# Optimization experiments

Hardware: AMD Instinct MI355X
Metric: run time of the kernel (lower is better)

Reference implementation:

```python
import jax, jax.numpy as jnp
import numpy as np

B, M, D, N, P = 8, 4096, 1024, 64, 2
TEMP = 0.1
EPS = 1e-12  # torch F.normalize default eps


def setup_inputs() -> dict:
    key = jax.random.key(0)
    k1, k2, k3 = jax.random.split(key, 3)
    x = jax.random.normal(k1, (B, M, D), jnp.float32)
    # xavier_normal_(phi, gain=1.5): std = 1.5*sqrt(2/(fan_in+fan_out)) with fan_in=D, fan_out=N*P
    phi = jax.random.normal(k2, (D, N, P), jnp.float32) * np.float32(1.5 * np.sqrt(2.0 / (D + N * P)))
    scale = jnp.ones((1,), jnp.float32)
    W = jax.random.normal(k3, (N, D, D), jnp.float32) * np.float32(1.0 / np.sqrt(D))
    b = jnp.zeros((N, D), jnp.float32)
    return {"x": x, "phi": phi, "scale": scale, "W": W, "b": b}


def reference(x, phi, scale, W, b):
    # normalize tokens along feature dim, phi along dim 0 (like F.normalize)
    xn = x / jnp.maximum(jnp.linalg.norm(x, axis=2, keepdims=True), EPS)
    phin = scale * (phi / jnp.maximum(jnp.linalg.norm(phi, axis=0, keepdims=True), EPS))
    # router logits [b, m, n, p]
    logits = jnp.einsum('bmd,dnp->bmnp', xn, phin) / TEMP
    d = jax.nn.softmax(logits, axis=1)                    # dispatch: softmax over tokens m
    c = jax.nn.softmax(logits.reshape(B, M, N * P), axis=-1).reshape(B, M, N, P)  # combine: softmax over (n,p)
    xs = jnp.einsum('bmd,bmnp->bnpd', x, d)               # slot inputs [b, n, p, d]
    # per-expert Linear(dim, dim): batched over expert axis n
    ys = jnp.einsum('bnpd,nde->bnpe', xs, W) + b[None, :, None, :]
    y = jnp.einsum('bnpd,bmnp->bmd', ys, c)
    return y + x  # add_residual=True
```

## Files before the change

kernel.cpp:

```cpp
#include <hip/hip_runtime.h>
#include <hip/hip_bf16.h>
#include <math.h>

#define B_ 8
#define M_ 4096
#define D_ 1024
#define NP_ 128
#define TEMP_ 0.1f
#define EPS_ 1e-12f

typedef __attribute__((ext_vector_type(8))) short bf16x8;
typedef __attribute__((ext_vector_type(4))) float f32x4;

__device__ __forceinline__ unsigned short f2bf(float f) {
    union { float f; unsigned int u; } v; v.f = f;
    unsigned int u = v.u;
    u += 0x7fff + ((u >> 16) & 1);
    return (unsigned short)(u >> 16);
}

__device__ __forceinline__ void stage_tile(const char* gbase, size_t row_stride,
                                           char* lds, int tid) {
    const int lane = tid & 63, w = tid >> 6;
#pragma unroll
    for (int t = 0; t < 2; ++t) {
        const int row = w * 32 + t * 16 + (lane >> 2);
        const char* g = gbase + (size_t)row * row_stride + (lane & 3) * 16;
        char* l = lds + (w * 32 + t * 16) * 64 + lane * 16;
        __builtin_amdgcn_global_load_lds((const __attribute__((address_space(1))) unsigned int*)g,
                                         (__attribute__((address_space(3))) unsigned int*)l,
                                         16, 0, 0);
    }
}

__device__ __forceinline__ void stage_rows64(const char* gbase, size_t row_stride,
                                             char* lds, int tid) {
    const int lane = tid & 63, w = tid >> 6;
    const int row = w * 16 + (lane >> 2);
    const char* g = gbase + (size_t)row * row_stride + (lane & 3) * 16;
    char* l = lds + (w * 16) * 64 + lane * 16;
    __builtin_amdgcn_global_load_lds((const __attribute__((address_space(1))) unsigned int*)g,
                                     (__attribute__((address_space(3))) unsigned int*)l,
                                     16, 0, 0);
}

template <int NI, int NJ>
__device__ __forceinline__ void mfma_tile(const char* At, const char* Bt,
                                          f32x4 (&acc)[NI][NJ], int wm, int wn,
                                          int fr, int q) {
    bf16x8 a[NI], bb[NJ];
#pragma unroll
    for (int i = 0; i < NI; ++i)
        a[i] = *(const bf16x8*)(At + (wm + i * 16 + fr) * 64 + q * 16);
#pragma unroll
    for (int j = 0; j < NJ; ++j)
        bb[j] = *(const bf16x8*)(Bt + (wn + j * 16 + fr) * 64 + q * 16);
#pragma unroll
    for (int i = 0; i < NI; ++i)
#pragma unroll
        for (int j = 0; j < NJ; ++j)
            acc[i][j] = __builtin_amdgcn_mfma_f32_16x16x32_bf16(a[i], bb[j], acc[i][j], 0, 0, 0);
}

__global__ __launch_bounds__(256) void k_prepT(const float* __restrict__ x,
                                               unsigned short* __restrict__ xbf,
                                               unsigned short* __restrict__ xbfT,
                                               float* __restrict__ rinv) {
    const int p = blockIdx.x;
    const int b = p >> 6, m0 = (p & 63) * 64;
    const int tid = threadIdx.x;
    const int mg = tid >> 4;
    const int d4 = tid & 15;
    __shared__ unsigned short lt[2][64][72];
    float ss[4] = {0.f, 0.f, 0.f, 0.f};
    for (int ch = 0; ch < 16; ++ch) {
        const int d0 = ch * 64;
        const int buf = ch & 1;
#pragma unroll
        for (int ii = 0; ii < 4; ++ii) {
            const int m = mg + ii * 16;
            float4 v = *(const float4*)(x + ((size_t)(b * M_ + m0 + m)) * D_ + d0 + d4 * 4);
            ss[ii] += v.x * v.x + v.y * v.y + v.z * v.z + v.w * v.w;
            ushort4 bv;
            bv.x = f2bf(v.x); bv.y = f2bf(v.y); bv.z = f2bf(v.z); bv.w = f2bf(v.w);
            *(ushort4*)(xbf + ((size_t)(b * M_ + m0 + m)) * D_ + d0 + d4 * 4) = bv;
            lt[buf][d4 * 4 + 0][m] = bv.x;
            lt[buf][d4 * 4 + 1][m] = bv.y;
            lt[buf][d4 * 4 + 2][m] = bv.z;
            lt[buf][d4 * 4 + 3][m] = bv.w;
        }
        __syncthreads();
        const int dl = tid >> 2, mq = (tid & 3) * 16;
        bf16x8 v0 = *(const bf16x8*)&lt[buf][dl][mq];
        bf16x8 v1 = *(const bf16x8*)&lt[buf][dl][mq + 8];
        unsigned short* to = xbfT + ((size_t)(b * D_ + d0 + dl)) * M_ + m0 + mq;
        *(bf16x8*)(to) = v0;
        *(bf16x8*)(to + 8) = v1;
    }
#pragma unroll
    for (int ii = 0; ii < 4; ++ii) {
        float s = ss[ii];
        s += __shfl_down(s, 8, 16);
        s += __shfl_down(s, 4, 16);
        s += __shfl_down(s, 2, 16);
        s += __shfl_down(s, 1, 16);
        if (d4 == 0)
            rinv[b * M_ + m0 + mg + ii * 16] = 1.0f / (fmaxf(sqrtf(s), EPS_) * TEMP_);
    }
}

__global__ void k_phin(const float* __restrict__ phi, const float* __restrict__ scale,
                       unsigned short* __restrict__ phinT) {
    const int np = blockIdx.x, tid = threadIdx.x;
    float ss = 0.f;
    for (int d = tid; d < D_; d += 256) {
        float v = phi[d * NP_ + np];
        ss += v * v;
    }
    __shared__ float red[256];
    red[tid] = ss;
    __syncthreads();
    for (int s = 128; s > 0; s >>= 1) {
        if (tid < s) red[tid] += red[tid + s];
        __syncthreads();
    }
    float inv = scale[0] / fmaxf(sqrtf(red[0]), EPS_);
    for (int d = tid; d < D_; d += 256) phinT[np * D_ + d] = f2bf(phi[d * NP_ + np] * inv);
}

__global__ __launch_bounds__(256) void k_logits(const unsigned short* __restrict__ phinT,
                                                const unsigned short* __restrict__ xbf,
                                                const float* __restrict__ rinv,
                                                float* __restrict__ logitsT) {
    const int b = blockIdx.y, m0 = blockIdx.x * 64;
    const int tid = threadIdx.x, lane = tid & 63, w = tid >> 6;
    __shared__ char At[2][8192], Bt[2][4096];
    f32x4 acc[4][2] = {};
    const char* abase = (const char*)phinT;
    const char* bbase = (const char*)(xbf + ((size_t)b * M_ + m0) * D_);
    const int wm = (w & 1) * 64, wn = (w >> 1) * 32;
    const int fr = lane & 15, q = lane >> 4;
    stage_tile(abase, 2048, At[0], tid);
    stage_rows64(bbase, 2048, Bt[0], tid);
    __syncthreads();
    int cur = 0;
    for (int k0 = 64; k0 < 2048; k0 += 64) {
        stage_tile(abase + k0, 2048, At[cur ^ 1], tid);
        stage_rows64(bbase + k0, 2048, Bt[cur ^ 1], tid);
        mfma_tile<4, 2>(At[cur], Bt[cur], acc, wm, wn, fr, q);
        __syncthreads();
        cur ^= 1;
    }
    mfma_tile<4, 2>(At[cur], Bt[cur], acc, wm, wn, fr, q);
#pragma unroll
    for (int j = 0; j < 2; ++j) {
        const int m = m0 + wn + j * 16 + fr;
        const float r = rinv[b * M_ + m];
#pragma unroll
        for (int i = 0; i < 4; ++i) {
            const int nprow = wm + i * 16 + q * 4;
#pragma unroll
            for (int reg = 0; reg < 4; ++reg)
                logitsT[((size_t)b * NP_ + nprow + reg) * M_ + m] = acc[i][j][reg] * r;
        }
    }
}

__global__ void k_colstats(const float* __restrict__ logitsT, float* __restrict__ cmax,
                           float* __restrict__ cinv) {
    const int row = blockIdx.x * 4 + (threadIdx.x >> 6);
    const int lane = threadIdx.x & 63;
    const float4* base = (const float4*)(logitsT + (size_t)row * M_);
    float mx = -1e30f, sm = 0.f;
#pragma unroll 4
    for (int it = 0; it < 16; ++it) {
        float4 v = base[lane + 64 * it];
        float lm = fmaxf(fmaxf(v.x, v.y), fmaxf(v.z, v.w));
        float nm = fmaxf(mx, lm);
        sm = sm * __expf(mx - nm) + __expf(v.x - nm) + __expf(v.y - nm) + __expf(v.z - nm) +
             __expf(v.w - nm);
        mx = nm;
    }
    for (int off = 32; off > 0; off >>= 1) {
        float om = __shfl_down(mx, off), os = __shfl_down(sm, off);
        float nm = fmaxf(mx, om);
        sm = sm * __expf(mx - nm) + os * __expf(om - nm);
        mx = nm;
    }
    if (lane == 0) {
        cmax[row] = mx;
        cinv[row] = 1.0f / sm;
    }
}

__global__ __launch_bounds__(256) void k_weights(const float* __restrict__ logitsT,
                                                 const float* __restrict__ cmax,
                                                 const float* __restrict__ cinv,
                                                 unsigned short* __restrict__ dvalT,
                                                 unsigned short* __restrict__ cbf) {
    const int b = blockIdx.y, m0 = blockIdx.x * 32;
    const int tid = threadIdx.x;
    __shared__ float lt[128][36];
    __shared__ float red[32][8];
    __shared__ float rstat[32][2];
    const int np = tid >> 1;
    const int mh = (tid & 1) * 16;
    const float cm = cmax[b * NP_ + np], ci = cinv[b * NP_ + np];
#pragma unroll
    for (int ii = 0; ii < 4; ++ii) {
        const int mq = mh + ii * 4;
        float4 v = *(const float4*)(logitsT + ((size_t)b * NP_ + np) * M_ + m0 + mq);
        *(float4*)&lt[np][mq] = v;
        ushort4 e;
        e.x = f2bf(__expf(v.x - cm) * ci);
        e.y = f2bf(__expf(v.y - cm) * ci);
        e.z = f2bf(__expf(v.z - cm) * ci);
        e.w = f2bf(__expf(v.w - cm) * ci);
        *(ushort4*)(dvalT + ((size_t)b * NP_ + np) * M_ + m0 + mq) = e;
    }
    __syncthreads();
    const int mm = tid >> 3, g = tid & 7;
    float mx = -1e30f;
#pragma unroll
    for (int i = 0; i < 16; ++i) mx = fmaxf(mx, lt[g * 16 + i][mm]);
    red[mm][g] = mx;
    __syncthreads();
    if (g == 0) {
        float M2 = red[mm][0];
#pragma unroll
        for (int k = 1; k < 8; ++k) M2 = fmaxf(M2, red[mm][k]);
        rstat[mm][0] = M2;
    }
    __syncthreads();
    const float rm = rstat[mm][0];
    float s = 0.f;
#pragma unroll
    for (int i = 0; i < 16; ++i) s += __expf(lt[g * 16 + i][mm] - rm);
    red[mm][g] = s;
    __syncthreads();
    if (g == 0) {
        float S = 0.f;
#pragma unroll
        for (int k = 0; k < 8; ++k) S += red[mm][k];
        rstat[mm][1] = 1.0f / S;
    }
    __syncthreads();
    const float ri = rstat[mm][1];
    bf16x8 o0, o1;
#pragma unroll
    for (int i = 0; i < 8; ++i) o0[i] = (short)f2bf(__expf(lt[g * 16 + i][mm] - rm) * ri);
#pragma unroll
    for (int i = 0; i < 8; ++i) o1[i] = (short)f2bf(__expf(lt[g * 16 + 8 + i][mm] - rm) * ri);
    unsigned short* co = cbf + ((size_t)b * M_ + m0 + mm) * NP_ + g * 16;
    *(bf16x8*)(co) = o0;
    *(bf16x8*)(co + 8) = o1;
}

__global__ __launch_bounds__(256) void k_xs(const unsigned short* __restrict__ dvalT,
                                            const unsigned short* __restrict__ xbfT,
                                            float* __restrict__ partial) {
    const int dt = blockIdx.x, kc = blockIdx.y, b = blockIdx.z;
    const int d0 = dt * 128;
    const int tid = threadIdx.x, lane = tid & 63, w = tid >> 6;
    __shared__ char At[2][8192], Bt[2][8192];
    f32x4 acc[4][4] = {};
    const char* abase = (const char*)(dvalT + (size_t)b * NP_ * M_) + (size_t)kc * 1024;
    const char* bbase = (const char*)(xbfT + ((size_t)b * D_ + d0) * M_) + (size_t)kc * 1024;
    const int wm = (w & 1) * 64, wn = (w >> 1) * 64;
    const int fr = lane & 15, q = lane >> 4;
    stage_tile(abase, (size_t)M_ * 2, At[0], tid);
    stage_tile(bbase, (size_t)M_ * 2, Bt[0], tid);
    __syncthreads();
    int cur = 0;
    for (int k0 = 64; k0 < 1024; k0 += 64) {
        stage_tile(abase + k0, (size_t)M_ * 2, At[cur ^ 1], tid);
        stage_tile(bbase + k0, (size_t)M_ * 2, Bt[cur ^ 1], tid);
        mfma_tile<4, 4>(At[cur], Bt[cur], acc, wm, wn, fr, q);
        __syncthreads();
        cur ^= 1;
    }
    mfma_tile<4, 4>(At[cur], Bt[cur], acc, wm, wn, fr, q);
#pragma unroll
    for (int j = 0; j < 4; ++j) {
        const int d = d0 + wn + j * 16 + fr;
#pragma unroll
        for (int i = 0; i < 4; ++i) {
            const int nprow = wm + i * 16 + q * 4;
#pragma unroll
            for (int reg = 0; reg < 4; ++reg)
                partial[(((size_t)kc * B_ + b) * NP_ + nprow + reg) * D_ + d] = acc[i][j][reg];
        }
    }
}

__global__ void k_xsred(const float* __restrict__ partial, float* __restrict__ xs) {
    const size_t i = ((size_t)blockIdx.x * 256 + threadIdx.x) * 4;
    const size_t CH = (size_t)B_ * NP_ * D_;
    float4 o = *(const float4*)(partial + i);
#pragma unroll
    for (int c = 1; c < 8; ++c) {
        float4 s = *(const float4*)(partial + (size_t)c * CH + i);
        o.x += s.x; o.y += s.y; o.z += s.z; o.w += s.w;
    }
    *(float4*)(xs + i) = o;
}

__global__ __launch_bounds__(256) void k_ys(const float* __restrict__ xs,
                                            const float* __restrict__ W,
                                            const float* __restrict__ bias,
                                            unsigned short* __restrict__ ysT) {
    const int et = blockIdx.x;
    const int n = blockIdx.y;
    const int e0 = et * 128;
    const int tid = threadIdx.x, tx = tid & 31, ty = tid >> 5;
    __shared__ float wt[32][128];
    __shared__ float xst[16][32];
    float acc[2][4];
#pragma unroll
    for (int j = 0; j < 2; ++j)
#pragma unroll
        for (int q = 0; q < 4; ++q) acc[j][q] = 0.f;
    const float* wbase = W + (size_t)n * D_ * D_;
    for (int k0 = 0; k0 < D_; k0 += 32) {
#pragma unroll
        for (int it = 0; it < 4; ++it) {
            int idx = tid + 256 * it;
            int row = idx >> 5, c4 = (idx & 31) * 4;
            *(float4*)(&wt[row][c4]) = *(const float4*)(wbase + (size_t)(k0 + row) * D_ + e0 + c4);
        }
        if (tid < 128) {
            int r = tid >> 3, c4 = (tid & 7) * 4;
            int bb = r >> 1, pp = r & 1;
            *(float4*)(&xst[r][c4]) =
                *(const float4*)(xs + ((size_t)bb * NP_ + n * 2 + pp) * D_ + k0 + c4);
        }
        __syncthreads();
#pragma unroll
        for (int k = 0; k < 32; ++k) {
            float4 w4 = *(const float4*)(&wt[k][tx * 4]);
            float r0 = xst[ty * 2][k], r1 = xst[ty * 2 + 1][k];
            acc[0][0] += r0 * w4.x; acc[0][1] += r0 * w4.y;
            acc[0][2] += r0 * w4.z; acc[0][3] += r0 * w4.w;
            acc[1][0] += r1 * w4.x; acc[1][1] += r1 * w4.y;
            acc[1][2] += r1 * w4.z; acc[1][3] += r1 * w4.w;
        }
        __syncthreads();
    }
    float4 bv = *(const float4*)(bias + n * D_ + e0 + tx * 4);
#pragma unroll
    for (int j = 0; j < 2; ++j) {
        const int r = ty * 2 + j;
        const int bb = r >> 1, pp = r & 1;
        float v0 = acc[j][0] + bv.x, v1 = acc[j][1] + bv.y;
        float v2 = acc[j][2] + bv.z, v3 = acc[j][3] + bv.w;
        ysT[((size_t)bb * D_ + e0 + tx * 4 + 0) * NP_ + n * 2 + pp] = f2bf(v0);
        ysT[((size_t)bb * D_ + e0 + tx * 4 + 1) * NP_ + n * 2 + pp] = f2bf(v1);
        ysT[((size_t)bb * D_ + e0 + tx * 4 + 2) * NP_ + n * 2 + pp] = f2bf(v2);
        ysT[((size_t)bb * D_ + e0 + tx * 4 + 3) * NP_ + n * 2 + pp] = f2bf(v3);
    }
}

__global__ __launch_bounds__(256) void k_final(const unsigned short* __restrict__ cbf,
                                               const unsigned short* __restrict__ ysT,
                                               const float* __restrict__ x,
                                               float* __restrict__ out) {
    const int et = blockIdx.x, mt = blockIdx.y, b = blockIdx.z;
    const int e0 = et * 128, m0 = mt * 128;
    const int tid = threadIdx.x, lane = tid & 63, w = tid >> 6;
    __shared__ char At[2][8192], Bt[2][8192];
    f32x4 acc[4][4] = {};
    const char* abase = (const char*)(cbf + ((size_t)b * M_ + m0) * NP_);
    const char* bbase = (const char*)(ysT + ((size_t)b * D_ + e0) * NP_);
    const int wm = (w & 1) * 64, wn = (w >> 1) * 64;
    const int fr = lane & 15, q = lane >> 4;
    stage_tile(abase, 256, At[0], tid);
    stage_tile(bbase, 256, Bt[0], tid);
    __syncthreads();
    int cur = 0;
    for (int k0 = 64; k0 < 256; k0 += 64) {
        stage_tile(abase + k0, 256, At[cur ^ 1], tid);
        stage_tile(bbase + k0, 256, Bt[cur ^ 1], tid);
        mfma_tile<4, 4>(At[cur], Bt[cur], acc, wm, wn, fr, q);
        __syncthreads();
        cur ^= 1;
    }
    mfma_tile<4, 4>(At[cur], Bt[cur], acc, wm, wn, fr, q);
#pragma unroll
    for (int i = 0; i < 4; ++i) {
#pragma unroll
        for (int reg = 0; reg < 4; ++reg) {
            const int m = m0 + wm + i * 16 + q * 4 + reg;
#pragma unroll
            for (int j = 0; j < 4; ++j) {
                const int e = e0 + wn + j * 16 + fr;
                const size_t idx = ((size_t)b * M_ + m) * D_ + e;
                out[idx] = acc[i][j][reg] + x[idx];
            }
        }
    }
}

extern "C" void kernel_launch(void* const* d_in, const int* in_sizes, int n_in,
                              void* d_out, int out_size, void* d_ws, size_t ws_size,
                              hipStream_t stream) {
    const float* x = (const float*)d_in[0];
    const float* phi = (const float*)d_in[1];
    const float* scale = (const float*)d_in[2];
    const float* W = (const float*)d_in[3];
    const float* bias = (const float*)d_in[4];
    float* out = (float*)d_out;

    char* ws = (char*)d_ws;
    float* rinv = (float*)ws;
    float* cmax = (float*)(ws + 131072);
    float* cinv = (float*)(ws + 135168);
    unsigned short* phinT = (unsigned short*)(ws + 139264);
    unsigned short* xbf = (unsigned short*)(ws + 401408);
    unsigned short* xbfT = (unsigned short*)(ws + 401408 + 67108864);
    float* logitsT = (float*)(ws + 401408 + 134217728);
    unsigned short* dvalT = (unsigned short*)(ws + 401408 + 150994944);
    unsigned short* cbf = (unsigned short*)(ws + 401408 + 159383552);
    float* partial = (float*)xbf;
    float* xs = (float*)((char*)xbf + 33554432);
    unsigned short* ysT = (unsigned short*)((char*)xbf + 37748736);

    k_prepT<<<512, 256, 0, stream>>>(x, xbf, xbfT, rinv);
    k_phin<<<128, 256, 0, stream>>>(phi, scale, phinT);
    k_logits<<<dim3(64, 8), 256, 0, stream>>>(phinT, xbf, rinv, logitsT);
    k_colstats<<<256, 256, 0, stream>>>(logitsT, cmax, cinv);
    k_weights<<<dim3(128, 8), 256, 0, stream>>>(logitsT, cmax, cinv, dvalT, cbf);
    k_xs<<<dim3(8, 8, 8), 256, 0, stream>>>(dvalT, xbfT, partial);
    k_xsred<<<1024, 256, 0, stream>>>(partial, xs);
    k_ys<<<dim3(8, 64), 256, 0, stream>>>(xs, W, bias, ysT);
    k_final<<<dim3(8, 32, 8), 256, 0, stream>>>(cbf, ysT, x, out);
}
```

Baseline: 661.1 us.

## Swap GEMM operand roles for vectorized float4 epilogue stores and split logits grid

```diff
diff --git a/kernel.cpp b/kernel.cpp
--- a/kernel.cpp
+++ b/kernel.cpp
@@ -132,36 +132,41 @@
                                                 const unsigned short* __restrict__ xbf,
                                                 const float* __restrict__ rinv,
                                                 float* __restrict__ logitsT) {
-    const int b = blockIdx.y, m0 = blockIdx.x * 64;
+    const int m0 = blockIdx.x * 64;
+    const int np0 = blockIdx.y * 64;
+    const int b = blockIdx.z;
     const int tid = threadIdx.x, lane = tid & 63, w = tid >> 6;
-    __shared__ char At[2][8192], Bt[2][4096];
-    f32x4 acc[4][2] = {};
-    const char* abase = (const char*)phinT;
-    const char* bbase = (const char*)(xbf + ((size_t)b * M_ + m0) * D_);
-    const int wm = (w & 1) * 64, wn = (w >> 1) * 32;
+    __shared__ char At[2][4096], Bt[2][4096];
+    f32x4 acc[2][2] = {};
+    const char* abase = (const char*)(xbf + ((size_t)b * M_ + m0) * D_);
+    const char* bbase = (const char*)(phinT + (size_t)np0 * D_);
+    const int wmm = (w & 1) * 32, wnn = (w >> 1) * 32;
     const int fr = lane & 15, q = lane >> 4;
-    stage_tile(abase, 2048, At[0], tid);
+    stage_rows64(abase, 2048, At[0], tid);
     stage_rows64(bbase, 2048, Bt[0], tid);
     __syncthreads();
     int cur = 0;
     for (int k0 = 64; k0 < 2048; k0 += 64) {
-        stage_tile(abase + k0, 2048, At[cur ^ 1], tid);
+        stage_rows64(abase + k0, 2048, At[cur ^ 1], tid);
         stage_rows64(bbase + k0, 2048, Bt[cur ^ 1], tid);
-        mfma_tile<4, 2>(At[cur], Bt[cur], acc, wm, wn, fr, q);
+        mfma_tile<2, 2>(At[cur], Bt[cur], acc, wmm, wnn, fr, q);
         __syncthreads();
         cur ^= 1;
     }
-    mfma_tile<4, 2>(At[cur], Bt[cur], acc, wm, wn, fr, q);
-#pragma unroll
-    for (int j = 0; j < 2; ++j) {
-        const int m = m0 + wn + j * 16 + fr;
-        const float r = rinv[b * M_ + m];
-#pragma unroll
-        for (int i = 0; i < 4; ++i) {
-            const int nprow = wm + i * 16 + q * 4;
-#pragma unroll
-            for (int reg = 0; reg < 4; ++reg)
-                logitsT[((size_t)b * NP_ + nprow + reg) * M_ + m] = acc[i][j][reg] * r;
+    mfma_tile<2, 2>(At[cur], Bt[cur], acc, wmm, wnn, fr, q);
+#pragma unroll
+    for (int i = 0; i < 2; ++i) {
+        const int mm = wmm + i * 16 + q * 4;
+        const float4 rv = *(const float4*)(rinv + (size_t)b * M_ + m0 + mm);
+#pragma unroll
+        for (int j = 0; j < 2; ++j) {
+            const int np = np0 + wnn + j * 16 + fr;
+            float4 o;
+            o.x = acc[i][j][0] * rv.x;
+            o.y = acc[i][j][1] * rv.y;
+            o.z = acc[i][j][2] * rv.z;
+            o.w = acc[i][j][3] * rv.w;
+            *(float4*)(logitsT + ((size_t)b * NP_ + np) * M_ + m0 + mm) = o;
         }
     }
 }
@@ -206,17 +211,21 @@
     const int np = tid >> 1;
     const int mh = (tid & 1) * 16;
     const float cm = cmax[b * NP_ + np], ci = cinv[b * NP_ + np];
+    unsigned short ev[16];
 #pragma unroll
     for (int ii = 0; ii < 4; ++ii) {
         const int mq = mh + ii * 4;
         float4 v = *(const float4*)(logitsT + ((size_t)b * NP_ + np) * M_ + m0 + mq);
         *(float4*)&lt[np][mq] = v;
-        ushort4 e;
-        e.x = f2bf(__expf(v.x - cm) * ci);
-        e.y = f2bf(__expf(v.y - cm) * ci);
-        e.z = f2bf(__expf(v.z - cm) * ci);
-        e.w = f2bf(__expf(v.w - cm) * ci);
-        *(ushort4*)(dvalT + ((size_t)b * NP_ + np) * M_ + m0 + mq) = e;
+        ev[ii * 4 + 0] = f2bf(__expf(v.x - cm) * ci);
+        ev[ii * 4 + 1] = f2bf(__expf(v.y - cm) * ci);
+        ev[ii * 4 + 2] = f2bf(__expf(v.z - cm) * ci);
+        ev[ii * 4 + 3] = f2bf(__expf(v.w - cm) * ci);
+    }
+    {
+        unsigned short* dp = dvalT + ((size_t)b * NP_ + np) * M_ + m0 + mh;
+        *(bf16x8*)dp = *(const bf16x8*)&ev[0];
+        *(bf16x8*)(dp + 8) = *(const bf16x8*)&ev[8];
     }
     __syncthreads();
     const int mm = tid >> 3, g = tid & 7;
@@ -260,35 +269,35 @@
                                             const unsigned short* __restrict__ xbfT,
                                             float* __restrict__ partial) {
     const int dt = blockIdx.x, kc = blockIdx.y, b = blockIdx.z;
-    const int d0 = dt * 128;
+    const int d0 = dt * 64;
     const int tid = threadIdx.x, lane = tid & 63, w = tid >> 6;
-    __shared__ char At[2][8192], Bt[2][8192];
-    f32x4 acc[4][4] = {};
-    const char* abase = (const char*)(dvalT + (size_t)b * NP_ * M_) + (size_t)kc * 1024;
-    const char* bbase = (const char*)(xbfT + ((size_t)b * D_ + d0) * M_) + (size_t)kc * 1024;
-    const int wm = (w & 1) * 64, wn = (w >> 1) * 64;
+    __shared__ char At[2][4096], Bt[2][8192];
+    f32x4 acc[2][4] = {};
+    const char* abase = (const char*)(xbfT + ((size_t)b * D_ + d0) * M_) + (size_t)kc * 1024;
+    const char* bbase = (const char*)(dvalT + (size_t)b * NP_ * M_) + (size_t)kc * 1024;
+    const int wmm = (w & 1) * 32, wnn = (w >> 1) * 64;
     const int fr = lane & 15, q = lane >> 4;
-    stage_tile(abase, (size_t)M_ * 2, At[0], tid);
+    stage_rows64(abase, (size_t)M_ * 2, At[0], tid);
     stage_tile(bbase, (size_t)M_ * 2, Bt[0], tid);
     __syncthreads();
     int cur = 0;
     for (int k0 = 64; k0 < 1024; k0 += 64) {
-        stage_tile(abase + k0, (size_t)M_ * 2, At[cur ^ 1], tid);
+        stage_rows64(abase + k0, (size_t)M_ * 2, At[cur ^ 1], tid);
         stage_tile(bbase + k0, (size_t)M_ * 2, Bt[cur ^ 1], tid);
-        mfma_tile<4, 4>(At[cur], Bt[cur], acc, wm, wn, fr, q);
+        mfma_tile<2, 4>(At[cur], Bt[cur], acc, wmm, wnn, fr, q);
         __syncthreads();
         cur ^= 1;
     }
-    mfma_tile<4, 4>(At[cur], Bt[cur], acc, wm, wn, fr, q);
-#pragma unroll
-    for (int j = 0; j < 4; ++j) {
-        const int d = d0 + wn + j * 16 + fr;
-#pragma unroll
-        for (int i = 0; i < 4; ++i) {
-            const int nprow = wm + i * 16 + q * 4;
-#pragma unroll
-            for (int reg = 0; reg < 4; ++reg)
-                partial[(((size_t)kc * B_ + b) * NP_ + nprow + reg) * D_ + d] = acc[i][j][reg];
+    mfma_tile<2, 4>(At[cur], Bt[cur], acc, wmm, wnn, fr, q);
+#pragma unroll
+    for (int i = 0; i < 2; ++i) {
+        const int dd = d0 + wmm + i * 16 + q * 4;
+#pragma unroll
+        for (int j = 0; j < 4; ++j) {
+            const int np = wnn + j * 16 + fr;
+            float4 o;
+            o.x = acc[i][j][0]; o.y = acc[i][j][1]; o.z = acc[i][j][2]; o.w = acc[i][j][3];
+            *(float4*)(partial + (((size_t)kc * B_ + b) * NP_ + np) * D_ + dd) = o;
         }
     }
 }
@@ -369,9 +378,9 @@
     const int tid = threadIdx.x, lane = tid & 63, w = tid >> 6;
     __shared__ char At[2][8192], Bt[2][8192];
     f32x4 acc[4][4] = {};
-    const char* abase = (const char*)(cbf + ((size_t)b * M_ + m0) * NP_);
-    const char* bbase = (const char*)(ysT + ((size_t)b * D_ + e0) * NP_);
-    const int wm = (w & 1) * 64, wn = (w >> 1) * 64;
+    const char* abase = (const char*)(ysT + ((size_t)b * D_ + e0) * NP_);
+    const char* bbase = (const char*)(cbf + ((size_t)b * M_ + m0) * NP_);
+    const int wmm = (w & 1) * 64, wnn = (w >> 1) * 64;
     const int fr = lane & 15, q = lane >> 4;
     stage_tile(abase, 256, At[0], tid);
     stage_tile(bbase, 256, Bt[0], tid);
@@ -380,22 +389,25 @@
     for (int k0 = 64; k0 < 256; k0 += 64) {
         stage_tile(abase + k0, 256, At[cur ^ 1], tid);
         stage_tile(bbase + k0, 256, Bt[cur ^ 1], tid);
-        mfma_tile<4, 4>(At[cur], Bt[cur], acc, wm, wn, fr, q);
+        mfma_tile<4, 4>(At[cur], Bt[cur], acc, wmm, wnn, fr, q);
         __syncthreads();
         cur ^= 1;
     }
-    mfma_tile<4, 4>(At[cur], Bt[cur], acc, wm, wn, fr, q);
+    mfma_tile<4, 4>(At[cur], Bt[cur], acc, wmm, wnn, fr, q);
 #pragma unroll
     for (int i = 0; i < 4; ++i) {
-#pragma unroll
-        for (int reg = 0; reg < 4; ++reg) {
-            const int m = m0 + wm + i * 16 + q * 4 + reg;
-#pragma unroll
-            for (int j = 0; j < 4; ++j) {
-                const int e = e0 + wn + j * 16 + fr;
-                const size_t idx = ((size_t)b * M_ + m) * D_ + e;
-                out[idx] = acc[i][j][reg] + x[idx];
-            }
+        const int e = e0 + wmm + i * 16 + q * 4;
+#pragma unroll
+        for (int j = 0; j < 4; ++j) {
+            const int m = m0 + wnn + j * 16 + fr;
+            const size_t idx = ((size_t)b * M_ + m) * D_ + e;
+            float4 xv = *(const float4*)(x + idx);
+            float4 o;
+            o.x = acc[i][j][0] + xv.x;
+            o.y = acc[i][j][1] + xv.y;
+            o.z = acc[i][j][2] + xv.z;
+            o.w = acc[i][j][3] + xv.w;
+            *(float4*)(out + idx) = o;
         }
     }
 }
@@ -426,10 +438,10 @@
 
     k_prepT<<<512, 256, 0, stream>>>(x, xbf, xbfT, rinv);
     k_phin<<<128, 256, 0, stream>>>(phi, scale, phinT);
-    k_logits<<<dim3(64, 8), 256, 0, stream>>>(phinT, xbf, rinv, logitsT);
+    k_logits<<<dim3(64, 2, 8), 256, 0, stream>>>(phinT, xbf, rinv, logitsT);
     k_colstats<<<256, 256, 0, stream>>>(logitsT, cmax, cinv);
     k_weights<<<dim3(128, 8), 256, 0, stream>>>(logitsT, cmax, cinv, dvalT, cbf);
-    k_xs<<<dim3(8, 8, 8), 256, 0, stream>>>(dvalT, xbfT, partial);
+    k_xs<<<dim3(16, 8, 8), 256, 0, stream>>>(dvalT, xbfT, partial);
     k_xsred<<<1024, 256, 0, stream>>>(partial, xs);
     k_ys<<<dim3(8, 64), 256, 0, stream>>>(xs, W, bias, ysT);
     k_final<<<dim3(8, 32, 8), 256, 0, stream>>>(cbf, ysT, x, out);
```

Result: slower. 694.0 us (+5.0%).
